# Optimization experiments

Measured on AMD Instinct MI355X. Metric: run time of the kernel, lower is better.

The kernel has to match this reference:

```python
import jax, jax.numpy as jnp
import numpy as np

B = 4096
FEAT = 40960
HID = 1024
L1 = 64
L2 = 32
P_ACTIVE = 30.0 / FEAT  # ~30 active features per position


def setup_inputs() -> dict:
    key = jax.random.key(0)
    ks = jax.random.split(key, 12)
    # Sparse binary HalfKP-style features
    white_features = (jax.random.uniform(ks[0], (B, FEAT)) < P_ACTIVE).astype(jnp.float32)
    black_features = (jax.random.uniform(ks[1], (B, FEAT)) < P_ACTIVE).astype(jnp.float32)
    stm = (jax.random.uniform(ks[2], (B, 1)) < 0.5).astype(jnp.float32)
    s = 0.02
    params = {
        'ft_w': jax.random.normal(ks[3], (HID, FEAT), jnp.float32) * s,
        'ft_b': jax.random.normal(ks[4], (HID,), jnp.float32) * s,
        'l1_w': jax.random.normal(ks[5], (L1, 2 * HID), jnp.float32) * s,
        'l1_b': jax.random.normal(ks[6], (L1,), jnp.float32) * s,
        'l2_w': jax.random.normal(ks[7], (L2, L1), jnp.float32) * s,
        'l2_b': jax.random.normal(ks[8], (L2,), jnp.float32) * s,
        'l3_w': jax.random.normal(ks[9], (1, L2), jnp.float32) * s,
        'l3_b': jax.random.normal(ks[10], (1,), jnp.float32) * s,
    }
    return dict(white_features=white_features, black_features=black_features, stm=stm, **params)


def reference(white_features, black_features, stm,
              ft_w, ft_b, l1_w, l1_b, l2_w, l2_b, l3_w, l3_b):
    # Feature transformer (shared weights, both perspectives)
    w = white_features @ ft_w.T + ft_b  # [B, HID]
    b = black_features @ ft_w.T + ft_b  # [B, HID]
    wb = jnp.concatenate([w, b], axis=1)  # [B, 2*HID]
    bw = jnp.concatenate([b, w], axis=1)
    acc = stm * wb + (1.0 - stm) * bw
    h1 = jnp.clip(acc, 0.0, 1.0)
    h2 = jnp.clip(h1 @ l1_w.T + l1_b, 0.0, 1.0)
    h3 = jnp.clip(h2 @ l2_w.T + l2_b, 0.0, 1.0)
    raw = h3 @ l3_w.T + l3_b  # [B, 1]
    return jax.nn.sigmoid(raw), raw
```

## Files before the change

kernel.cpp:

```cpp
#include <hip/hip_runtime.h>
#include <hip/hip_bf16.h>

#define B_SZ 4096
#define FEAT 40960
#define HID  1024
#define L1N  64
#define L2N  32
#define IDX_CAP 128
#define ROWS 4

static __device__ __forceinline__ unsigned short f2bf(float x) {
    __hip_bfloat16 h = __float2bfloat16(x);
    return *reinterpret_cast<unsigned short*>(&h);
}
static __device__ __forceinline__ float bf2f(unsigned short u) {
    return __uint_as_float(((unsigned int)u) << 16);
}
static __device__ __forceinline__ float bf2f_lo(unsigned int u) {
    return __uint_as_float(u << 16);
}
static __device__ __forceinline__ float bf2f_hi(unsigned int u) {
    return __uint_as_float(u & 0xffff0000u);
}
static __device__ __forceinline__ unsigned int packbf(float lo, float hi) {
    return (unsigned int)f2bf(lo) | ((unsigned int)f2bf(hi) << 16);
}
static __device__ __forceinline__ float clipf(float x) {
    return fminf(fmaxf(x, 0.0f), 1.0f);
}

__global__ __launch_bounds__(256) void transpose_ftw(
    const float* __restrict__ ftw, unsigned short* __restrict__ ftwT) {
    __shared__ float tile[32][65];
    const int tx = threadIdx.x;
    const int ty = threadIdx.y;
    const int f0 = blockIdx.x * 32;
    const int h0 = blockIdx.y * 64;
#pragma unroll
    for (int i = 0; i < 8; ++i) {
        int h = ty + 8 * i;
        tile[tx][h] = ftw[(size_t)(h0 + h) * FEAT + f0 + tx];
    }
    __syncthreads();
#pragma unroll
    for (int i = 0; i < 4; ++i) {
        int f = ty + 8 * i;
        unsigned int pk = packbf(tile[f][2 * tx], tile[f][2 * tx + 1]);
        ((unsigned int*)(ftwT + (size_t)(f0 + f) * HID + h0))[tx] = pk;
    }
}

__global__ __launch_bounds__(256) void scan_gather(
    const float* __restrict__ wf, const float* __restrict__ bfeat,
    const float* __restrict__ stm, const unsigned short* __restrict__ ftwT,
    const float* __restrict__ ftb, unsigned int* __restrict__ h1) {

    __shared__ int idxs[2][IDX_CAP];
    __shared__ int cnts[2];

    const int t = threadIdx.x;
    const int row = blockIdx.x;

    if (t < 2) cnts[t] = 0;
    __syncthreads();

#pragma unroll
    for (int pp = 0; pp < 2; ++pp) {
        const float4* s4 = (const float4*)((pp ? bfeat : wf) + (size_t)row * FEAT);
#pragma unroll 4
        for (int it = 0; it < (FEAT / 4) / 256; ++it) {
            int i4 = it * 256 + t;
            float4 v = s4[i4];
            int base = i4 * 4;
            if (v.x != 0.f) { int p = atomicAdd(&cnts[pp], 1); if (p < IDX_CAP) idxs[pp][p] = base + 0; }
            if (v.y != 0.f) { int p = atomicAdd(&cnts[pp], 1); if (p < IDX_CAP) idxs[pp][p] = base + 1; }
            if (v.z != 0.f) { int p = atomicAdd(&cnts[pp], 1); if (p < IDX_CAP) idxs[pp][p] = base + 2; }
            if (v.w != 0.f) { int p = atomicAdd(&cnts[pp], 1); if (p < IDX_CAP) idxs[pp][p] = base + 3; }
        }
    }
    __syncthreads();

    const int nw = min(cnts[0], IDX_CAP);
    const int nb = min(cnts[1], IDX_CAP);
    float4 bias = ((const float4*)ftb)[t];
    float aw0 = bias.x, aw1 = bias.y, aw2 = bias.z, aw3 = bias.w;
    float ab0 = bias.x, ab1 = bias.y, ab2 = bias.z, ab3 = bias.w;

#pragma unroll 4
    for (int i = 0; i < nw; ++i) {
        int f = idxs[0][i];
        ushort4 u = ((const ushort4*)(ftwT + (size_t)f * HID))[t];
        aw0 += bf2f(u.x); aw1 += bf2f(u.y); aw2 += bf2f(u.z); aw3 += bf2f(u.w);
    }
#pragma unroll 4
    for (int i = 0; i < nb; ++i) {
        int f = idxs[1][i];
        ushort4 u = ((const ushort4*)(ftwT + (size_t)f * HID))[t];
        ab0 += bf2f(u.x); ab1 += bf2f(u.y); ab2 += bf2f(u.z); ab3 += bf2f(u.w);
    }

    const bool wfirst = (stm[row] != 0.0f);
    float f0 = wfirst ? aw0 : ab0, f1 = wfirst ? aw1 : ab1;
    float f2 = wfirst ? aw2 : ab2, f3 = wfirst ? aw3 : ab3;
    float s0 = wfirst ? ab0 : aw0, s1 = wfirst ? ab1 : aw1;
    float s2 = wfirst ? ab2 : aw2, s3 = wfirst ? ab3 : aw3;

    uint2 pf, ps;
    pf.x = packbf(clipf(f0), clipf(f1)); pf.y = packbf(clipf(f2), clipf(f3));
    ps.x = packbf(clipf(s0), clipf(s1)); ps.y = packbf(clipf(s2), clipf(s3));

    unsigned int* dst = h1 + (size_t)row * (2 * HID / 2);
    ((uint2*)dst)[t]                 = pf;
    ((uint2*)(dst + HID / 2 * 1))[t + 0] = ps;
}

__global__ __launch_bounds__(256) void mlp_kernel(
    const unsigned int* __restrict__ h1,
    const float* __restrict__ l1w, const float* __restrict__ l1b,
    const float* __restrict__ l2w, const float* __restrict__ l2b,
    const float* __restrict__ l3w, const float* __restrict__ l3b,
    float* __restrict__ out) {

    __shared__ unsigned int h1p[ROWS][HID];
    __shared__ float4 part[4 * L1N];
    __shared__ float h2s[ROWS][L1N];
    __shared__ float h3s[ROWS][L2N];

    const int t = threadIdx.x;
    const int r0 = blockIdx.x * ROWS;

    {
        const uint4* src = (const uint4*)(h1 + (size_t)r0 * HID);
        uint4* dst = (uint4*)&h1p[0][0];
#pragma unroll
        for (int i = 0; i < 4; ++i) dst[i * 256 + t] = src[i * 256 + t];
    }
    __syncthreads();

    {
        const int k = t & 63, p = t >> 6;
        float a0 = 0.f, a1 = 0.f, a2 = 0.f, a3 = 0.f;
        const float4* w4 = (const float4*)(l1w + (size_t)k * 2 * HID + (size_t)p * 512);
        const int qbase = p * 256;
        for (int jj = 0; jj < 128; ++jj) {
            float4 w = w4[jj];
            int q = qbase + 2 * jj;
            unsigned int u00 = h1p[0][q], u01 = h1p[0][q + 1];
            unsigned int u10 = h1p[1][q], u11 = h1p[1][q + 1];
            unsigned int u20 = h1p[2][q], u21 = h1p[2][q + 1];
            unsigned int u30 = h1p[3][q], u31 = h1p[3][q + 1];
            a0 += w.x * bf2f_lo(u00) + w.y * bf2f_hi(u00) + w.z * bf2f_lo(u01) + w.w * bf2f_hi(u01);
            a1 += w.x * bf2f_lo(u10) + w.y * bf2f_hi(u10) + w.z * bf2f_lo(u11) + w.w * bf2f_hi(u11);
            a2 += w.x * bf2f_lo(u20) + w.y * bf2f_hi(u20) + w.z * bf2f_lo(u21) + w.w * bf2f_hi(u21);
            a3 += w.x * bf2f_lo(u30) + w.y * bf2f_hi(u30) + w.z * bf2f_lo(u31) + w.w * bf2f_hi(u31);
        }
        part[p * L1N + k] = make_float4(a0, a1, a2, a3);
    }
    __syncthreads();
    if (t < L1N) {
        float4 s0 = part[t], s1 = part[L1N + t], s2 = part[2 * L1N + t], s3 = part[3 * L1N + t];
        float b1 = l1b[t];
        h2s[0][t] = clipf(s0.x + s1.x + s2.x + s3.x + b1);
        h2s[1][t] = clipf(s0.y + s1.y + s2.y + s3.y + b1);
        h2s[2][t] = clipf(s0.z + s1.z + s2.z + s3.z + b1);
        h2s[3][t] = clipf(s0.w + s1.w + s2.w + s3.w + b1);
    }
    __syncthreads();

    if (t < ROWS * L2N) {
        int r = t >> 5, k2 = t & 31;
        float a = l2b[k2];
        for (int j = 0; j < L1N; ++j) a += h2s[r][j] * l2w[k2 * L1N + j];
        h3s[r][k2] = clipf(a);
    }
    __syncthreads();

    if (t < ROWS) {
        float raw = l3b[0];
        for (int j = 0; j < L2N; ++j) raw += h3s[t][j] * l3w[j];
        out[r0 + t] = 1.0f / (1.0f + expf(-raw));
        out[B_SZ + r0 + t] = raw;
    }
}

extern "C" void kernel_launch(void* const* d_in, const int* in_sizes, int n_in,
                              void* d_out, int out_size, void* d_ws, size_t ws_size,
                              hipStream_t stream) {
    const float* wf    = (const float*)d_in[0];
    const float* bfeat = (const float*)d_in[1];
    const float* stm   = (const float*)d_in[2];
    const float* ftw   = (const float*)d_in[3];
    const float* ftb   = (const float*)d_in[4];
    const float* l1w   = (const float*)d_in[5];
    const float* l1b   = (const float*)d_in[6];
    const float* l2w   = (const float*)d_in[7];
    const float* l2b   = (const float*)d_in[8];
    const float* l3w   = (const float*)d_in[9];
    const float* l3b   = (const float*)d_in[10];
    float* out = (float*)d_out;

    unsigned short* ftwT = (unsigned short*)d_ws;
    unsigned int* h1 = (unsigned int*)(ftwT + (size_t)FEAT * HID);

    transpose_ftw<<<dim3(FEAT / 32, HID / 64), dim3(32, 8), 0, stream>>>(ftw, ftwT);
    scan_gather<<<B_SZ, 256, 0, stream>>>(wf, bfeat, stm, ftwT, ftb, h1);
    mlp_kernel<<<B_SZ / ROWS, 256, 0, stream>>>(h1, l1w, l1b, l2w, l2b, l3w, l3b, out);
}
```

Before: 1.451 ms.

## Store transposed feature weights as scaled fp8 and fuse gather with MLP

The transposed feature-transformer weights are now stored as fp8 (e4m3) scaled by 64 instead of bf16, which halves the bytes written by the transpose and read by the gather. The gather kernel and the MLP kernel are fused into one per-row kernel, so the h1 activations stay in shared memory and no longer round-trip through global memory. Feature scans use nontemporal loads. In exchange, fp8 weights lose precision, and the MLP weights are now reloaded once per row instead of once per four rows.

```diff
diff --git a/kernel.cpp b/kernel.cpp
--- a/kernel.cpp
+++ b/kernel.cpp
@@ -7,14 +7,15 @@
 #define L1N  64
 #define L2N  32
 #define IDX_CAP 128
-#define ROWS 4
+#define W_SCALE 64.0f
+#define W_INV   0.015625f
+
+typedef float floatx2 __attribute__((ext_vector_type(2)));
+typedef float floatx4 __attribute__((ext_vector_type(4)));
 
 static __device__ __forceinline__ unsigned short f2bf(float x) {
     __hip_bfloat16 h = __float2bfloat16(x);
     return *reinterpret_cast<unsigned short*>(&h);
-}
-static __device__ __forceinline__ float bf2f(unsigned short u) {
-    return __uint_as_float(((unsigned int)u) << 16);
 }
 static __device__ __forceinline__ float bf2f_lo(unsigned int u) {
     return __uint_as_float(u << 16);
@@ -29,34 +30,47 @@
     return fminf(fmaxf(x, 0.0f), 1.0f);
 }
 
-__global__ __launch_bounds__(256) void transpose_ftw(
-    const float* __restrict__ ftw, unsigned short* __restrict__ ftwT) {
+__global__ __launch_bounds__(256) void transpose_fp8(
+    const float* __restrict__ ftw, unsigned char* __restrict__ ftwT8) {
     __shared__ float tile[32][65];
-    const int tx = threadIdx.x;
-    const int ty = threadIdx.y;
-    const int f0 = blockIdx.x * 32;
-    const int h0 = blockIdx.y * 64;
+    const int t  = threadIdx.x;
+    const int tx = t & 31;
+    const int ty = t >> 5;
+    const int f0 = (blockIdx.x % (FEAT / 32)) * 32;
+    const int h0 = (blockIdx.x / (FEAT / 32)) * 64;
 #pragma unroll
     for (int i = 0; i < 8; ++i) {
         int h = ty + 8 * i;
-        tile[tx][h] = ftw[(size_t)(h0 + h) * FEAT + f0 + tx];
+        tile[tx][h] = ftw[(size_t)(h0 + h) * FEAT + f0 + tx] * W_SCALE;
     }
     __syncthreads();
+    if (tx < 16) {
 #pragma unroll
-    for (int i = 0; i < 4; ++i) {
-        int f = ty + 8 * i;
-        unsigned int pk = packbf(tile[f][2 * tx], tile[f][2 * tx + 1]);
-        ((unsigned int*)(ftwT + (size_t)(f0 + f) * HID + h0))[tx] = pk;
+        for (int i = 0; i < 4; ++i) {
+            int f = ty + 8 * i;
+            unsigned int pk = 0;
+            pk = __builtin_amdgcn_cvt_pk_fp8_f32(tile[f][4 * tx + 0], tile[f][4 * tx + 1], pk, false);
+            pk = __builtin_amdgcn_cvt_pk_fp8_f32(tile[f][4 * tx + 2], tile[f][4 * tx + 3], pk, true);
+            ((unsigned int*)(ftwT8 + (size_t)(f0 + f) * HID + h0))[tx] = pk;
+        }
     }
 }
 
-__global__ __launch_bounds__(256) void scan_gather(
+__global__ __launch_bounds__(256) void nnue_row(
     const float* __restrict__ wf, const float* __restrict__ bfeat,
-    const float* __restrict__ stm, const unsigned short* __restrict__ ftwT,
-    const float* __restrict__ ftb, unsigned int* __restrict__ h1) {
+    const float* __restrict__ stm, const unsigned char* __restrict__ ftwT8,
+    const float* __restrict__ ftb,
+    const float* __restrict__ l1w, const float* __restrict__ l1b,
+    const float* __restrict__ l2w, const float* __restrict__ l2b,
+    const float* __restrict__ l3w, const float* __restrict__ l3b,
+    float* __restrict__ out) {
 
     __shared__ int idxs[2][IDX_CAP];
     __shared__ int cnts[2];
+    __shared__ unsigned int h1p[HID];
+    __shared__ float part[4 * L1N];
+    __shared__ float h2s[L1N];
+    __shared__ float h3s[L2N];
 
     const int t = threadIdx.x;
     const int row = blockIdx.x;
@@ -66,11 +80,11 @@
 
 #pragma unroll
     for (int pp = 0; pp < 2; ++pp) {
-        const float4* s4 = (const float4*)((pp ? bfeat : wf) + (size_t)row * FEAT);
+        const floatx4* s4 = (const floatx4*)((pp ? bfeat : wf) + (size_t)row * FEAT);
 #pragma unroll 4
         for (int it = 0; it < (FEAT / 4) / 256; ++it) {
             int i4 = it * 256 + t;
-            float4 v = s4[i4];
+            floatx4 v = __builtin_nontemporal_load(&s4[i4]);
             int base = i4 * 4;
             if (v.x != 0.f) { int p = atomicAdd(&cnts[pp], 1); if (p < IDX_CAP) idxs[pp][p] = base + 0; }
             if (v.y != 0.f) { int p = atomicAdd(&cnts[pp], 1); if (p < IDX_CAP) idxs[pp][p] = base + 1; }
@@ -83,103 +97,76 @@
     const int nw = min(cnts[0], IDX_CAP);
     const int nb = min(cnts[1], IDX_CAP);
     float4 bias = ((const float4*)ftb)[t];
-    float aw0 = bias.x, aw1 = bias.y, aw2 = bias.z, aw3 = bias.w;
-    float ab0 = bias.x, ab1 = bias.y, ab2 = bias.z, ab3 = bias.w;
+    float aw0 = bias.x * W_SCALE, aw1 = bias.y * W_SCALE;
+    float aw2 = bias.z * W_SCALE, aw3 = bias.w * W_SCALE;
+    float ab0 = aw0, ab1 = aw1, ab2 = aw2, ab3 = aw3;
 
 #pragma unroll 4
     for (int i = 0; i < nw; ++i) {
-        int f = idxs[0][i];
-        ushort4 u = ((const ushort4*)(ftwT + (size_t)f * HID))[t];
-        aw0 += bf2f(u.x); aw1 += bf2f(u.y); aw2 += bf2f(u.z); aw3 += bf2f(u.w);
+        unsigned int u = ((const unsigned int*)(ftwT8 + (size_t)idxs[0][i] * HID))[t];
+        floatx2 lo = __builtin_amdgcn_cvt_pk_f32_fp8(u, false);
+        floatx2 hi = __builtin_amdgcn_cvt_pk_f32_fp8(u, true);
+        aw0 += lo.x; aw1 += lo.y; aw2 += hi.x; aw3 += hi.y;
     }
 #pragma unroll 4
     for (int i = 0; i < nb; ++i) {
-        int f = idxs[1][i];
-        ushort4 u = ((const ushort4*)(ftwT + (size_t)f * HID))[t];
-        ab0 += bf2f(u.x); ab1 += bf2f(u.y); ab2 += bf2f(u.z); ab3 += bf2f(u.w);
+        unsigned int u = ((const unsigned int*)(ftwT8 + (size_t)idxs[1][i] * HID))[t];
+        floatx2 lo = __builtin_amdgcn_cvt_pk_f32_fp8(u, false);
+        floatx2 hi = __builtin_amdgcn_cvt_pk_f32_fp8(u, true);
+        ab0 += lo.x; ab1 += lo.y; ab2 += hi.x; ab3 += hi.y;
     }
 
-    const bool wfirst = (stm[row] != 0.0f);
-    float f0 = wfirst ? aw0 : ab0, f1 = wfirst ? aw1 : ab1;
-    float f2 = wfirst ? aw2 : ab2, f3 = wfirst ? aw3 : ab3;
-    float s0 = wfirst ? ab0 : aw0, s1 = wfirst ? ab1 : aw1;
-    float s2 = wfirst ? ab2 : aw2, s3 = wfirst ? ab3 : aw3;
-
-    uint2 pf, ps;
-    pf.x = packbf(clipf(f0), clipf(f1)); pf.y = packbf(clipf(f2), clipf(f3));
-    ps.x = packbf(clipf(s0), clipf(s1)); ps.y = packbf(clipf(s2), clipf(s3));
-
-    unsigned int* dst = h1 + (size_t)row * (2 * HID / 2);
-    ((uint2*)dst)[t]                 = pf;
-    ((uint2*)(dst + HID / 2 * 1))[t + 0] = ps;
-}
-
-__global__ __launch_bounds__(256) void mlp_kernel(
-    const unsigned int* __restrict__ h1,
-    const float* __restrict__ l1w, const float* __restrict__ l1b,
-    const float* __restrict__ l2w, const float* __restrict__ l2b,
-    const float* __restrict__ l3w, const float* __restrict__ l3b,
-    float* __restrict__ out) {
-
-    __shared__ unsigned int h1p[ROWS][HID];
-    __shared__ float4 part[4 * L1N];
-    __shared__ float h2s[ROWS][L1N];
-    __shared__ float h3s[ROWS][L2N];
-
-    const int t = threadIdx.x;
-    const int r0 = blockIdx.x * ROWS;
-
     {
-        const uint4* src = (const uint4*)(h1 + (size_t)r0 * HID);
-        uint4* dst = (uint4*)&h1p[0][0];
-#pragma unroll
-        for (int i = 0; i < 4; ++i) dst[i * 256 + t] = src[i * 256 + t];
+        const bool wfirst = (stm[row] != 0.0f);
+        float f0 = (wfirst ? aw0 : ab0) * W_INV, f1 = (wfirst ? aw1 : ab1) * W_INV;
+        float f2 = (wfirst ? aw2 : ab2) * W_INV, f3 = (wfirst ? aw3 : ab3) * W_INV;
+        float s0 = (wfirst ? ab0 : aw0) * W_INV, s1 = (wfirst ? ab1 : aw1) * W_INV;
+        float s2 = (wfirst ? ab2 : aw2) * W_INV, s3 = (wfirst ? ab3 : aw3) * W_INV;
+        h1p[2 * t]           = packbf(clipf(f0), clipf(f1));
+        h1p[2 * t + 1]       = packbf(clipf(f2), clipf(f3));
+        h1p[512 + 2 * t]     = packbf(clipf(s0), clipf(s1));
+        h1p[512 + 2 * t + 1] = packbf(clipf(s2), clipf(s3));
     }
     __syncthreads();
 
     {
         const int k = t & 63, p = t >> 6;
-        float a0 = 0.f, a1 = 0.f, a2 = 0.f, a3 = 0.f;
+        float a = 0.f;
         const float4* w4 = (const float4*)(l1w + (size_t)k * 2 * HID + (size_t)p * 512);
         const int qbase = p * 256;
         for (int jj = 0; jj < 128; ++jj) {
             float4 w = w4[jj];
             int q = qbase + 2 * jj;
-            unsigned int u00 = h1p[0][q], u01 = h1p[0][q + 1];
-            unsigned int u10 = h1p[1][q], u11 = h1p[1][q + 1];
-            unsigned int u20 = h1p[2][q], u21 = h1p[2][q + 1];
-            unsigned int u30 = h1p[3][q], u31 = h1p[3][q + 1];
-            a0 += w.x * bf2f_lo(u00) + w.y * bf2f_hi(u00) + w.z * bf2f_lo(u01) + w.w * bf2f_hi(u01);
-            a1 += w.x * bf2f_lo(u10) + w.y * bf2f_hi(u10) + w.z * bf2f_lo(u11) + w.w * bf2f_hi(u11);
-            a2 += w.x * bf2f_lo(u20) + w.y * bf2f_hi(u20) + w.z * bf2f_lo(u21) + w.w * bf2f_hi(u21);
-            a3 += w.x * bf2f_lo(u30) + w.y * bf2f_hi(u30) + w.z * bf2f_lo(u31) + w.w * bf2f_hi(u31);
+            unsigned int u0 = h1p[q], u1 = h1p[q + 1];
+            a += w.x * bf2f_lo(u0) + w.y * bf2f_hi(u0) + w.z * bf2f_lo(u1) + w.w * bf2f_hi(u1);
         }
-        part[p * L1N + k] = make_float4(a0, a1, a2, a3);
+        part[p * L1N + k] = a;
     }
     __syncthreads();
     if (t < L1N) {
-        float4 s0 = part[t], s1 = part[L1N + t], s2 = part[2 * L1N + t], s3 = part[3 * L1N + t];
-        float b1 = l1b[t];
-        h2s[0][t] = clipf(s0.x + s1.x + s2.x + s3.x + b1);
-        h2s[1][t] = clipf(s0.y + s1.y + s2.y + s3.y + b1);
-        h2s[2][t] = clipf(s0.z + s1.z + s2.z + s3.z + b1);
-        h2s[3][t] = clipf(s0.w + s1.w + s2.w + s3.w + b1);
+        h2s[t] = clipf(part[t] + part[L1N + t] + part[2 * L1N + t] + part[3 * L1N + t] + l1b[t]);
     }
     __syncthreads();
 
-    if (t < ROWS * L2N) {
-        int r = t >> 5, k2 = t & 31;
-        float a = l2b[k2];
-        for (int j = 0; j < L1N; ++j) a += h2s[r][j] * l2w[k2 * L1N + j];
-        h3s[r][k2] = clipf(a);
+    if (t < L2N) {
+        float a = l2b[t];
+        const float4* w4 = (const float4*)(l2w + t * L1N);
+        const float4* h4 = (const float4*)h2s;
+#pragma unroll
+        for (int j = 0; j < L1N / 4; ++j) {
+            float4 w = w4[j]; float4 h = h4[j];
+            a += w.x * h.x + w.y * h.y + w.z * h.z + w.w * h.w;
+        }
+        h3s[t] = clipf(a);
     }
     __syncthreads();
 
-    if (t < ROWS) {
+    if (t == 0) {
         float raw = l3b[0];
-        for (int j = 0; j < L2N; ++j) raw += h3s[t][j] * l3w[j];
-        out[r0 + t] = 1.0f / (1.0f + expf(-raw));
-        out[B_SZ + r0 + t] = raw;
+#pragma unroll
+        for (int j = 0; j < L2N; ++j) raw += h3s[j] * l3w[j];
+        out[row] = 1.0f / (1.0f + expf(-raw));
+        out[B_SZ + row] = raw;
     }
 }
 
@@ -199,10 +186,9 @@
     const float* l3b   = (const float*)d_in[10];
     float* out = (float*)d_out;
 
-    unsigned short* ftwT = (unsigned short*)d_ws;
-    unsigned int* h1 = (unsigned int*)(ftwT + (size_t)FEAT * HID);
+    unsigned char* ftwT8 = (unsigned char*)d_ws;
 
-    transpose_ftw<<<dim3(FEAT / 32, HID / 64), dim3(32, 8), 0, stream>>>(ftw, ftwT);
-    scan_gather<<<B_SZ, 256, 0, stream>>>(wf, bfeat, stm, ftwT, ftb, h1);
-    mlp_kernel<<<B_SZ / ROWS, 256, 0, stream>>>(h1, l1w, l1b, l2w, l2b, l3w, l3b, out);
+    transpose_fp8<<<(FEAT / 32) * (HID / 64), 256, 0, stream>>>(ftw, ftwT8);
+    nnue_row<<<B_SZ, 256, 0, stream>>>(wf, bfeat, stm, ftwT8, ftb,
+                                       l1w, l1b, l2w, l2b, l3w, l3b, out);
 }
```

After: 1.528 ms. 5.3% more time.
